# Performance work log

Hardware: AMD Instinct MI355X
Metric: run time of the kernel (lower is better)

Reference implementation:

```python
import jax, jax.numpy as jnp
import numpy as np
from jax import lax

BS, C, H, W = 512, 256, 6, 6
NS, NOC, OD, ROUTE = 32, 10, 16, 3  # num_shared, num_out_caps, out_dim, route_num


def setup_inputs() -> dict:
    key = jax.random.key(0)
    k1, k2, k3, k4 = jax.random.split(key, 4)
    x = jax.random.normal(k1, (BS, C, H, W), jnp.float32)
    target = jax.random.randint(k2, (BS,), 0, 10, jnp.int32)  # unused (look_into_details=False)
    W_conv = jax.random.normal(k3, (NS * NOC * OD, C // NS, 1, 1), jnp.float32) * 0.05
    b_conv = jax.random.normal(k4, (NS * NOC * OD,), jnp.float32) * 0.05
    return {"x": x, "target": target, "W_conv": W_conv, "b_conv": b_conv}


def _capsule_forward(x, W_conv, b_conv):
    bs = x.shape[0]
    # grouped 1x1 conv: [bs, NS*NOC*OD, h, w]
    raw = lax.conv_general_dilated(
        x, W_conv, window_strides=(1, 1), padding='VALID',
        dimension_numbers=('NCHW', 'OIHW', 'NCHW'), feature_group_count=NS)
    raw = raw + b_conv[None, :, None, None]
    h, w = raw.shape[2], raw.shape[3]
    # pred (u_hat): [bs, num_in_caps, num_out_caps, out_dim]
    pred = raw.reshape(bs, NS, NOC, OD, h, w).transpose(0, 1, 4, 5, 2, 3)
    pred = pred.reshape(bs, NS * h * w, NOC, OD)
    b = jnp.zeros((bs, NOC, NS * h * w), x.dtype)  # routing logits
    v = None
    for _ in range(ROUTE):
        c = jax.nn.softmax(b, axis=1)                  # softmax over out-caps axis
        s = jnp.einsum('bji,bijd->bjd', c, pred)       # i=in caps, j=out caps
        norm = jnp.linalg.norm(s, axis=2, keepdims=True)
        v = s * (norm / (1.0 + norm * norm))           # squash: n^2/(1+n^2) * s/n
        delta_b = lax.stop_gradient(jnp.einsum('bjd,bijd->bji', v, pred))
        b = b + delta_b
    return v  # [bs, NOC, OD]


def reference(x, target, W_conv, b_conv):
    return _capsule_forward(x, W_conv, b_conv)
```

## Files before the change

kernel.cpp:

```cpp
#include <hip/hip_runtime.h>
#include <hip/hip_fp16.h>
#include <math.h>


#define BSZ   512
#define C_IN  256
#define HW    36
#define NS    32
#define NOC   10
#define OD    16
#define ROUTE 3
#define NIC   1152
#define NT    640
#define EROW  12

typedef __half2 h2;

__device__ __forceinline__ h2 u2h(unsigned int v) {
    union { unsigned int u; h2 h; } x; x.u = v; return x.h;
}
__device__ __forceinline__ h2 shflx_h2(h2 v, int m) {
    union { h2 h; int i; } x; x.h = v; x.i = __shfl_xor(x.i, m); return x.h;
}

__global__ __launch_bounds__(256) void convert_w(
    const float* __restrict__ Wc, const float* __restrict__ bc,
    __half* __restrict__ w16)
{
    const int n = 40960 + 5120;
    for (int i = blockIdx.x * 256 + threadIdx.x; i < n; i += gridDim.x * 256) {
        float v = (i < 40960) ? Wc[i] : bc[i - 40960];
        w16[i] = __float2half(v);
    }
}

__global__ __launch_bounds__(NT, 2) void caps_kernel(
    const float*  __restrict__ x,
    const __half* __restrict__ w16,
    const __half* __restrict__ bc16,
    float* __restrict__ out)
{
    __shared__ h2 xs[NIC * 4];
    __shared__ unsigned short eL[NIC * EROW];

    const int tid = threadIdx.x;
    const float* xb = x + (size_t)blockIdx.x * (C_IN * HW);

    for (int t5 = tid; t5 < 9 * 128; t5 += NT) {
        int p4 = t5 >> 7, c2 = t5 & 127;
        int nsc = c2 >> 2, k2 = c2 & 3;
        const float* s0 = xb + (2 * c2) * HW + p4 * 4;
        float4 a = *(const float4*)s0;
        float4 b = *(const float4*)(s0 + HW);
        xs[((p4 * 4 + 0) * 32 + nsc) * 4 + k2] = __floats2half2_rn(a.x, b.x);
        xs[((p4 * 4 + 1) * 32 + nsc) * 4 + k2] = __floats2half2_rn(a.y, b.y);
        xs[((p4 * 4 + 2) * 32 + nsc) * 4 + k2] = __floats2half2_rn(a.z, b.z);
        xs[((p4 * 4 + 3) * 32 + nsc) * 4 + k2] = __floats2half2_rn(a.w, b.w);
    }
    __syncthreads();

    const int j     = tid >> 6;
    const int dhalf = (tid >> 5) & 1;
    const int ns    = tid & 31;

    const __half* wbase = w16 + (size_t)(ns * 160 + j * 16 + dhalf * 8) * 8;
    float bcv[8];
    {
        uint4 bv = *(const uint4*)(bc16 + ns * 160 + j * 16 + dhalf * 8);
        float2 b0 = __half22float2(u2h(bv.x));
        float2 b1 = __half22float2(u2h(bv.y));
        float2 b2 = __half22float2(u2h(bv.z));
        float2 b3 = __half22float2(u2h(bv.w));
        bcv[0]=b0.x; bcv[1]=b0.y; bcv[2]=b1.x; bcv[3]=b1.y;
        bcv[4]=b2.x; bcv[5]=b2.y; bcv[6]=b3.x; bcv[7]=b3.y;
    }

    const int q0 = dhalf * 9;
    float ua[9];
    h2    ua2[4];

    for (int it = 0; it < ROUTE; ++it) {
        h2 t2[4];
        h2 zz = __float2half2_rn(0.f);
        t2[0] = zz; t2[1] = zz; t2[2] = zz; t2[3] = zz;
        float tc = 0.f;
        if (it == 0) {
            #pragma unroll
            for (int q = 0; q < 9; ++q) {
                #pragma unroll
                for (int s = 0; s < 2; ++s) {
                    int row = (2 * (q0 + q) + s) * 32 + ns;
                    uint4 xv = *(const uint4*)&xs[row * 4];
                    t2[0] = __hadd2(t2[0], u2h(xv.x));
                    t2[1] = __hadd2(t2[1], u2h(xv.y));
                    t2[2] = __hadd2(t2[2], u2h(xv.z));
                    t2[3] = __hadd2(t2[3], u2h(xv.w));
                }
            }
            h2 tenth = __float2half2_rn(0.1f);
            #pragma unroll
            for (int k = 0; k < 4; ++k) t2[k] = __hmul2(t2[k], tenth);
            tc = 1.8f;
        } else {
            #pragma unroll
            for (int q = 0; q < 9; ++q) {
                #pragma unroll
                for (int s = 0; s < 2; ++s) {
                    int row = (2 * (q0 + q) + s) * 32 + ns;
                    uint4 xv = *(const uint4*)&xs[row * 4];
                    h2 x0 = u2h(xv.x), x1 = u2h(xv.y), x2 = u2h(xv.z), x3 = u2h(xv.w);
                    h2 a = __hmul2(ua2[0], x0);
                    a = __hfma2(ua2[1], x1, a);
                    a = __hfma2(ua2[2], x2, a);
                    a = __hfma2(ua2[3], x3, a);
                    float2 af = __half22float2(a);
                    float bb = ua[8] + af.x + af.y;
                    float sv = *(const float*)&eL[row * EROW + 10];
                    float c = __expf(bb) * sv;
                    h2 c2 = __float2half2_rn(c);
                    t2[0] = __hfma2(c2, x0, t2[0]);
                    t2[1] = __hfma2(c2, x1, t2[1]);
                    t2[2] = __hfma2(c2, x2, t2[2]);
                    t2[3] = __hfma2(c2, x3, t2[3]);
                    tc += c;
                }
            }
        }
        #pragma unroll
        for (int k = 0; k < 4; ++k) t2[k] = __hadd2(t2[k], shflx_h2(t2[k], 32));
        tc += __shfl_xor(tc, 32);

        float ps[8];
        #pragma unroll
        for (int dd = 0; dd < 8; ++dd) {
            uint4 wv = *(const uint4*)(wbase + (size_t)dd * 8);
            h2 a = __hmul2(u2h(wv.x), t2[0]);
            a = __hfma2(u2h(wv.y), t2[1], a);
            a = __hfma2(u2h(wv.z), t2[2], a);
            a = __hfma2(u2h(wv.w), t2[3], a);
            float2 f = __half22float2(a);
            ps[dd] = f.x + f.y + bcv[dd] * tc;
        }
        #pragma unroll
        for (int mk = 1; mk < 32; mk <<= 1) {
            #pragma unroll
            for (int dd = 0; dd < 8; ++dd)
                ps[dd] += __shfl_xor(ps[dd], mk);
        }
        float ssp = 0.f;
        #pragma unroll
        for (int dd = 0; dd < 8; ++dd) ssp += ps[dd] * ps[dd];
        float ss = ssp + __shfl_xor(ssp, 32);
        float fc = sqrtf(ss) / (1.f + ss);

        if (it == ROUTE - 1) {
            if (ns == 0) {
                float* o = out + (size_t)blockIdx.x * (NOC * OD) + j * OD + dhalf * 8;
                *(float4*)o       = make_float4(ps[0]*fc, ps[1]*fc, ps[2]*fc, ps[3]*fc);
                *(float4*)(o + 4) = make_float4(ps[4]*fc, ps[5]*fc, ps[6]*fc, ps[7]*fc);
            }
            break;
        }

        h2 u2[4];
        u2[0] = zz; u2[1] = zz; u2[2] = zz; u2[3] = zz;
        float u8 = 0.f;
        #pragma unroll
        for (int dd = 0; dd < 8; ++dd) {
            float vv = ps[dd] * fc;
            h2 v2 = __float2half2_rn(vv);
            uint4 wv = *(const uint4*)(wbase + (size_t)dd * 8);
            u2[0] = __hfma2(v2, u2h(wv.x), u2[0]);
            u2[1] = __hfma2(v2, u2h(wv.y), u2[1]);
            u2[2] = __hfma2(v2, u2h(wv.z), u2[2]);
            u2[3] = __hfma2(v2, u2h(wv.w), u2[3]);
            u8 += vv * bcv[dd];
        }
        #pragma unroll
        for (int k = 0; k < 4; ++k) u2[k] = __hadd2(u2[k], shflx_h2(u2[k], 32));
        u8 += __shfl_xor(u8, 32);
        {
            float2 f0 = __half22float2(u2[0]);
            float2 f1 = __half22float2(u2[1]);
            float2 f2 = __half22float2(u2[2]);
            float2 f3 = __half22float2(u2[3]);
            if (it == 0) {
                ua[0]=f0.x; ua[1]=f0.y; ua[2]=f1.x; ua[3]=f1.y;
                ua[4]=f2.x; ua[5]=f2.y; ua[6]=f3.x; ua[7]=f3.y; ua[8]=u8;
            } else {
                ua[0]+=f0.x; ua[1]+=f0.y; ua[2]+=f1.x; ua[3]+=f1.y;
                ua[4]+=f2.x; ua[5]+=f2.y; ua[6]+=f3.x; ua[7]+=f3.y; ua[8]+=u8;
            }
            ua2[0] = __floats2half2_rn(ua[0], ua[1]);
            ua2[1] = __floats2half2_rn(ua[2], ua[3]);
            ua2[2] = __floats2half2_rn(ua[4], ua[5]);
            ua2[3] = __floats2half2_rn(ua[6], ua[7]);
        }

        #pragma unroll
        for (int q = 0; q < 9; ++q) {
            #pragma unroll
            for (int s = 0; s < 2; ++s) {
                int row = (2 * (q0 + q) + s) * 32 + ns;
                uint4 xv = *(const uint4*)&xs[row * 4];
                h2 a = __hmul2(ua2[0], u2h(xv.x));
                a = __hfma2(ua2[1], u2h(xv.y), a);
                a = __hfma2(ua2[2], u2h(xv.z), a);
                a = __hfma2(ua2[3], u2h(xv.w), a);
                float2 af = __half22float2(a);
                float bb = ua[8] + af.x + af.y;
                eL[row * EROW + j] = __half_as_ushort(__float2half_rn(__expf(bb)));
            }
        }
        __syncthreads();

        for (int i = tid; i < NIC; i += NT) {
            const h2* er = (const h2*)&eL[i * EROW];
            h2 sA = __hadd2(__hadd2(er[0], er[1]), __hadd2(er[2], er[3]));
            sA = __hadd2(sA, er[4]);
            float2 sf = __half22float2(sA);
            *(float*)&eL[i * EROW + 10] = __frcp_rn(sf.x + sf.y);
        }
        __syncthreads();
    }
}

extern "C" void kernel_launch(void* const* d_in, const int* in_sizes, int n_in,
                              void* d_out, int out_size, void* d_ws, size_t ws_size,
                              hipStream_t stream) {
    const float* x  = (const float*)d_in[0];
    const float* Wc = (const float*)d_in[2];
    const float* bc = (const float*)d_in[3];
    float* out = (float*)d_out;

    __half* w16 = (__half*)d_ws;
    convert_w<<<dim3(48), dim3(256), 0, stream>>>(Wc, bc, w16);
    caps_kernel<<<dim3(BSZ), dim3(NT), 0, stream>>>(x, w16, w16 + 40960, out);
}
```

Measured before the change: 104.5 us.

## Keep routing exponentials in registers and restructure softmax denominator layout

Each thread now keeps its computed exp(b) values in registers (packed half2 per pair of positions) and reuses them in the next routing iteration. This removes recomputing the logit dot product and exp in the s-accumulation loop. The shared exp buffer is relaid out as [out-cap][position][lane] so the denominator pass reads and writes conflict-free and runs over 576 threads, each handling two positions, with reciprocals stored in a float array. The cost is 9 extra registers per thread and a different reduction order in half precision.

```diff
diff --git a/kernel.cpp b/kernel.cpp
--- a/kernel.cpp
+++ b/kernel.cpp
@@ -12,7 +12,6 @@
 #define ROUTE 3
 #define NIC   1152
 #define NT    640
-#define EROW  12
 
 typedef __half2 h2;
 
@@ -40,8 +39,9 @@
     const __half* __restrict__ bc16,
     float* __restrict__ out)
 {
-    __shared__ h2 xs[NIC * 4];
-    __shared__ unsigned short eL[NIC * EROW];
+    __shared__ h2    xs[NIC * 4];
+    __shared__ h2    eJ[NOC * 18 * 32];
+    __shared__ float sinv2[NIC];
 
     const int tid = threadIdx.x;
     const float* xb = x + (size_t)blockIdx.x * (C_IN * HW);
@@ -78,6 +78,7 @@
     const int q0 = dhalf * 9;
     float ua[9];
     h2    ua2[4];
+    h2    ereg[9];
 
     for (int it = 0; it < ROUTE; ++it) {
         h2 t2[4];
@@ -104,25 +105,27 @@
         } else {
             #pragma unroll
             for (int q = 0; q < 9; ++q) {
-                #pragma unroll
-                for (int s = 0; s < 2; ++s) {
-                    int row = (2 * (q0 + q) + s) * 32 + ns;
-                    uint4 xv = *(const uint4*)&xs[row * 4];
-                    h2 x0 = u2h(xv.x), x1 = u2h(xv.y), x2 = u2h(xv.z), x3 = u2h(xv.w);
-                    h2 a = __hmul2(ua2[0], x0);
-                    a = __hfma2(ua2[1], x1, a);
-                    a = __hfma2(ua2[2], x2, a);
-                    a = __hfma2(ua2[3], x3, a);
-                    float2 af = __half22float2(a);
-                    float bb = ua[8] + af.x + af.y;
-                    float sv = *(const float*)&eL[row * EROW + 10];
-                    float c = __expf(bb) * sv;
-                    h2 c2 = __float2half2_rn(c);
-                    t2[0] = __hfma2(c2, x0, t2[0]);
-                    t2[1] = __hfma2(c2, x1, t2[1]);
-                    t2[2] = __hfma2(c2, x2, t2[2]);
-                    t2[3] = __hfma2(c2, x3, t2[3]);
-                    tc += c;
+                int pr = q0 + q;
+                float2 sv = *(const float2*)&sinv2[pr * 64 + ns * 2];
+                float2 ef = __half22float2(ereg[q]);
+                float c0 = ef.x * sv.x;
+                float c1 = ef.y * sv.y;
+                tc += c0 + c1;
+                h2 c20 = __float2half2_rn(c0);
+                h2 c21 = __float2half2_rn(c1);
+                {
+                    uint4 xv = *(const uint4*)&xs[((2 * pr + 0) * 32 + ns) * 4];
+                    t2[0] = __hfma2(c20, u2h(xv.x), t2[0]);
+                    t2[1] = __hfma2(c20, u2h(xv.y), t2[1]);
+                    t2[2] = __hfma2(c20, u2h(xv.z), t2[2]);
+                    t2[3] = __hfma2(c20, u2h(xv.w), t2[3]);
+                }
+                {
+                    uint4 xv = *(const uint4*)&xs[((2 * pr + 1) * 32 + ns) * 4];
+                    t2[0] = __hfma2(c21, u2h(xv.x), t2[0]);
+                    t2[1] = __hfma2(c21, u2h(xv.y), t2[1]);
+                    t2[2] = __hfma2(c21, u2h(xv.z), t2[2]);
+                    t2[3] = __hfma2(c21, u2h(xv.w), t2[3]);
                 }
             }
         }
@@ -199,27 +202,33 @@
 
         #pragma unroll
         for (int q = 0; q < 9; ++q) {
+            int pr = q0 + q;
+            float eb[2];
             #pragma unroll
             for (int s = 0; s < 2; ++s) {
-                int row = (2 * (q0 + q) + s) * 32 + ns;
+                int row = (2 * pr + s) * 32 + ns;
                 uint4 xv = *(const uint4*)&xs[row * 4];
                 h2 a = __hmul2(ua2[0], u2h(xv.x));
                 a = __hfma2(ua2[1], u2h(xv.y), a);
                 a = __hfma2(ua2[2], u2h(xv.z), a);
                 a = __hfma2(ua2[3], u2h(xv.w), a);
                 float2 af = __half22float2(a);
-                float bb = ua[8] + af.x + af.y;
-                eL[row * EROW + j] = __half_as_ushort(__float2half_rn(__expf(bb)));
-            }
+                eb[s] = __expf(ua[8] + af.x + af.y);
+            }
+            ereg[q] = __floats2half2_rn(eb[0], eb[1]);
+            eJ[(j * 18 + pr) * 32 + ns] = ereg[q];
         }
         __syncthreads();
 
-        for (int i = tid; i < NIC; i += NT) {
-            const h2* er = (const h2*)&eL[i * EROW];
-            h2 sA = __hadd2(__hadd2(er[0], er[1]), __hadd2(er[2], er[3]));
-            sA = __hadd2(sA, er[4]);
-            float2 sf = __half22float2(sA);
-            *(float*)&eL[i * EROW + 10] = __frcp_rn(sf.x + sf.y);
+        if (tid < 576) {
+            int pr = tid >> 5, a = tid & 31;
+            h2 s2 = eJ[pr * 32 + a];
+            #pragma unroll
+            for (int jj = 1; jj < NOC; ++jj)
+                s2 = __hadd2(s2, eJ[(jj * 18 + pr) * 32 + a]);
+            float2 sf = __half22float2(s2);
+            *(float2*)&sinv2[pr * 64 + a * 2] =
+                make_float2(__frcp_rn(sf.x), __frcp_rn(sf.y));
         }
         __syncthreads();
     }
```

Measured after the change: 100.5 us. 3.9% less time.
